# Performance work log

Measured on AMD Instinct MI355X. Metric: run time of the kernel, lower is better.

## Reference

```python
import jax, jax.numpy as jnp
import numpy as np

N, E, B, NC, NCAND, TOK, TITLE, V, GD = 10000, 200000, 64, 50, 5, 38, 30, 50000, 300
H, DH = 20, 20
D = H * DH  # news_dim = 400
NEG = -1e9


def setup_inputs() -> dict:
    key = jax.random.key(0)
    ks = jax.random.split(key, 24)
    s = lambda k, shape, sc=0.02: (jax.random.normal(k, shape, jnp.float32) * sc)
    return dict(
        subgraph_x=jax.random.randint(ks[0], (N, TOK), 0, V, jnp.int32),
        edge_index=jax.random.randint(ks[1], (2, E), 0, N, jnp.int32),
        # -1 marks padded click slots, as in the torch module
        mapping_idx=jax.random.randint(ks[2], (B, NC), -1, N, jnp.int32),
        candidate_news=jax.random.randint(ks[3], (B, NCAND, TOK), 0, V, jnp.int32),
        fake_candidate_news=jax.random.randint(ks[4], (B, NCAND, TOK), 0, V, jnp.int32),
        label=jnp.zeros((B,), jnp.int32),
        glove_emb=s(ks[5], (V, GD), 0.1),
        n_wq=s(ks[6], (GD, D)), n_wk=s(ks[7], (GD, D)), n_wv=s(ks[8], (GD, D)),
        n_wp=s(ks[9], (D, 200)), n_qp=s(ks[10], (200,)),
        ggc_w=s(ks[11], (3, D, D)),
        gru_wih=s(ks[12], (D, 3 * D)), gru_whh=s(ks[13], (D, 3 * D)),
        gru_bih=jnp.zeros((3 * D,), jnp.float32), gru_bhh=jnp.zeros((3 * D,), jnp.float32),
        w_click=s(ks[14], (2 * D, D)), b_click=jnp.zeros((D,), jnp.float32),
        u_wq=s(ks[15], (D, D)), u_wk=s(ks[16], (D, D)), u_wv=s(ks[17], (D, D)),
        u_wp=s(ks[18], (D, 200)), u_qp=s(ks[19], (200,)),
    )


def reference(subgraph_x, edge_index, mapping_idx, candidate_news, fake_candidate_news,
              label, glove_emb, n_wq, n_wk, n_wv, n_wp, n_qp, ggc_w, gru_wih, gru_whh,
              gru_bih, gru_bhh, w_click, b_click, u_wq, u_wk, u_wv, u_wp, u_qp):
    inv_sqrt = 1.0 / np.sqrt(DH).astype(np.float32)

    def news_encode(tokens):  # [..., TITLE] int -> [..., D]
        emb = glove_emb[tokens]                               # [..., T, GD]
        hd = emb.shape[:-1] + (H, DH)
        q = (emb @ n_wq).reshape(hd)
        k = (emb @ n_wk).reshape(hd)
        v = (emb @ n_wv).reshape(hd)
        att = jax.nn.softmax(jnp.einsum('...qhd,...khd->...hqk', q, k) * inv_sqrt, axis=-1)
        out = jnp.einsum('...hqk,...khd->...qhd', att, v).reshape(emb.shape[:-1] + (D,))
        a = jax.nn.softmax(jnp.tanh(out @ n_wp) @ n_qp, axis=-1)  # attention pooling over tokens
        return jnp.einsum('...t,...td->...d', a, out)

    # ---- process_news: encode every node once ----
    x_encoded = news_encode(subgraph_x[:, :TITLE])            # [N, D]
    mask = mapping_idx >= 0                                   # [B, NC]
    midx = jnp.where(mask, mapping_idx, 0)
    clicked_origin = x_encoded[midx] * mask[..., None]        # gather + masked_fill -> [B, NC, D]

    # ---- server: GatedGraphConv(D, num_layers=3, aggr='add') ----
    src, dst = edge_index[0], edge_index[1]
    h = x_encoded
    for l in range(3):
        m = h @ ggc_w[l]
        agg = jax.ops.segment_sum(m[src], dst, num_segments=x_encoded.shape[0])
        gi = agg @ gru_wih + gru_bih
        gh = h @ gru_whh + gru_bhh
        i_r, i_z, i_n = jnp.split(gi, 3, axis=-1)
        h_r, h_z, h_n = jnp.split(gh, 3, axis=-1)
        r = jax.nn.sigmoid(i_r + h_r)
        z = jax.nn.sigmoid(i_z + h_z)
        n = jnp.tanh(i_n + r * h_n)
        h = (1.0 - z) * n + z * h
    clicked_graph = h[midx] * mask[..., None]                 # [B, NC, D]

    # ---- click encoder: combine origin + graph views ----
    clicked_total = jnp.concatenate([clicked_origin, clicked_graph], -1) @ w_click + b_click  # [B,NC,D]

    # ---- user encoder: masked MHSA + masked attention pooling ----
    bsz, nc = clicked_total.shape[:2]
    q = (clicked_total @ u_wq).reshape(bsz, nc, H, DH)
    k = (clicked_total @ u_wk).reshape(bsz, nc, H, DH)
    v = (clicked_total @ u_wv).reshape(bsz, nc, H, DH)
    bias = jnp.where(mask, 0.0, NEG)                          # [B, NC]
    att = jax.nn.softmax(jnp.einsum('bqhd,bkhd->bhqk', q, k) * inv_sqrt + bias[:, None, None, :], axis=-1)
    out = jnp.einsum('bhqk,bkhd->bqhd', att, v).reshape(bsz, nc, D)
    pa = jax.nn.softmax(jnp.tanh(out @ u_wp) @ u_qp + bias, axis=-1)
    user_emb = jnp.einsum('bt,btd->bd', pa, out)              # [B, D]

    # ---- candidate encoding + dot-product scoring ----
    def score_cand(cand):
        c = news_encode(cand[..., :TITLE])                    # [B, NCAND, D]
        return jnp.einsum('bcd,bd->bc', c, user_emb)

    score_real = score_cand(candidate_news)
    score_fake = score_cand(fake_candidate_news)

    # ---- security loss: NCE (cross-entropy) + fake-uniformity penalty ----
    lsm = jax.nn.log_softmax(score_real, axis=-1)
    loss_real = -jnp.mean(jnp.take_along_axis(lsm, label[:, None], axis=1))
    loss_fake = -jnp.mean(jax.nn.log_softmax(score_fake, axis=-1))
    loss = 1.0 * loss_real + 0.5 * loss_fake
    return loss, score_real, score_fake
```

## Files before the change

### kernel.cpp

```cpp
#include <hip/hip_runtime.h>
#include <cmath>

#define NN 10000
#define EE 200000
#define BB 64
#define NCK 50
#define NCAND 5
#define TOKS 38
#define TITLE 30
#define GDIM 300
#define HH 20
#define DHD 20
#define DD 400
#define PP 200

typedef __attribute__((ext_vector_type(8))) short bh8;
typedef __attribute__((ext_vector_type(4))) float f32x4;

__device__ __forceinline__ float bf2f(unsigned short u) {
    return __uint_as_float(((unsigned int)u) << 16);
}
__device__ __forceinline__ unsigned short f2bf(float f) {
    unsigned int u = __float_as_uint(f);
    u += 0x7fffu + ((u >> 16) & 1u);
    return (unsigned short)(u >> 16);
}

__global__ __launch_bounds__(256) void prep_wt(
    const float* __restrict__ wq, const float* __restrict__ wk,
    const float* __restrict__ wv, unsigned short* __restrict__ Wt)
{
    int i = blockIdx.x * 256 + threadIdx.x;
    if (i >= 1200 * 320) return;
    int n = i / 320, k = i % 320;
    int m = n / 400, nn = n % 400;
    const float* W = (m == 0) ? wq : ((m == 1) ? wk : wv);
    float v = (k < GDIM) ? W[(size_t)k * DD + nn] : 0.f;
    Wt[i] = f2bf(v);
}

__global__ __launch_bounds__(256) void prep_wpt(
    const float* __restrict__ wp, unsigned short* __restrict__ wpT)
{
    int i = blockIdx.x * 256 + threadIdx.x;
    if (i >= 208 * 416) return;
    int n = i / 416, k = i % 416;
    float v = (n < PP && k < DD) ? wp[(size_t)k * PP + n] : 0.f;
    wpT[i] = f2bf(v);
}

__global__ __launch_bounds__(256) void prep_wgg(
    const float* __restrict__ ggc, unsigned short* __restrict__ wggT)
{
    int i = blockIdx.x * 256 + threadIdx.x;
    if (i >= 3 * 400 * 424) return;
    int l = i / (400*424), rem = i % (400*424);
    int n = rem / 424, k = rem % 424;
    float v = (k < DD) ? ggc[(size_t)l*DD*DD + (size_t)k*DD + n] : 0.f;
    wggT[i] = f2bf(v);
}

__global__ __launch_bounds__(256) void prep_gruw(
    const float* __restrict__ wih, const float* __restrict__ whh,
    unsigned short* __restrict__ wihT, unsigned short* __restrict__ whhT)
{
    int i = blockIdx.x * 256 + threadIdx.x;
    if (i >= 1200 * 424) return;
    int n = i / 424, k = i % 424;
    wihT[i] = f2bf((k < DD) ? wih[(size_t)k*1200 + n] : 0.f);
    whhT[i] = f2bf((k < DD) ? whh[(size_t)k*1200 + n] : 0.f);
}

__global__ __launch_bounds__(256) void news_enc(
    const int* __restrict__ sub_x,
    const int* __restrict__ cand,
    const int* __restrict__ fcand,
    const float* __restrict__ glove,
    const unsigned short* __restrict__ Wt,
    const unsigned short* __restrict__ wpT,
    const float* __restrict__ qp,
    float* __restrict__ x_enc,
    float* __restrict__ crnc,
    float* __restrict__ cfnc)
{
    __shared__ __align__(16) unsigned short uS[12288];
    __shared__ __align__(16) unsigned short outS[32*408 + 16];
    __shared__ int   tokS[32];
    __shared__ float alphaS[32];

    float* poolP = (float*)uS;

    const int tid  = threadIdx.x;
    const int item = blockIdx.x;
    const int w    = tid >> 6;
    const int lane = tid & 63;
    const int g    = lane >> 4;
    const int l15  = lane & 15;

    const int* tsrc; float* odst;
    if (item < NN) {
        tsrc = sub_x + (size_t)item * TOKS;
        odst = x_enc + (size_t)item * DD;
    } else if (item < NN + BB*NCAND) {
        int li = item - NN;
        tsrc = cand + (size_t)li * TOKS;
        odst = crnc + (size_t)li * DD;
    } else {
        int li = item - NN - BB*NCAND;
        tsrc = fcand + (size_t)li * TOKS;
        odst = cfnc + (size_t)li * DD;
    }

    if (tid < TITLE) tokS[tid] = tsrc[tid];
    for (int i = tid; i < 12288/2; i += 256) ((unsigned int*)uS)[i] = 0u;
    for (int i = tid; i < (32*408+16)/2; i += 256) ((unsigned int*)outS)[i] = 0u;
    __syncthreads();

    for (int i = tid; i < TITLE * 75; i += 256) {
        int t = i / 75, g4 = i % 75;
        const float4 v = *(const float4*)&glove[(size_t)tokS[t] * GDIM + g4 * 4];
        uS[t*328 + g4*4+0] = f2bf(v.x);
        uS[t*328 + g4*4+1] = f2bf(v.y);
        uS[t*328 + g4*4+2] = f2bf(v.z);
        uS[t*328 + g4*4+3] = f2bf(v.w);
    }
    __syncthreads();

    bh8 afr[2][10];
    #pragma unroll
    for (int mt = 0; mt < 2; ++mt)
        #pragma unroll
        for (int ks = 0; ks < 10; ++ks)
            afr[mt][ks] = *(const bh8*)&uS[(mt*16 + l15)*328 + ks*32 + g*8];
    __syncthreads();

    for (int i = tid; i < 12288/2; i += 256) ((unsigned int*)uS)[i] = 0u;
    __syncthreads();

    const float sc = 0.2236067977f;

    for (int hg = 0; hg < 5; ++hg) {
        {
            unsigned short* qme = uS + w*1024;
            for (int i = lane; i < 32*6; i += 64) {
                int r = i / 6, c = 20 + (i % 6) * 2;
                *(unsigned int*)&qme[r*32 + c] = 0u;
            }
        }

        #pragma unroll
        for (int tp = 0; tp < 2; ++tp) {
            const int ta = w*4 + tp*2, tb = ta + 1;
            const bool va_ = (ta < 15), vb_ = (tb < 15);
            const int tca = va_ ? ta : 0, tcb = vb_ ? tb : 0;
            const int ma = tca / 5, loca = tca % 5;
            const int mb = tcb / 5, locb = tcb % 5;
            const unsigned short* wba =
                Wt + (size_t)(ma*400 + hg*80 + loca*16 + l15) * 320;
            const unsigned short* wbb =
                Wt + (size_t)(mb*400 + hg*80 + locb*16 + l15) * 320;
            bh8 ba[10], bbf[10];
            #pragma unroll
            for (int ks = 0; ks < 10; ++ks) {
                ba[ks]  = *(const bh8*)&wba[ks*32 + g*8];
                bbf[ks] = *(const bh8*)&wbb[ks*32 + g*8];
            }
            __builtin_amdgcn_sched_barrier(0);
            f32x4 ca0 = {0.f,0.f,0.f,0.f}, ca1 = {0.f,0.f,0.f,0.f};
            f32x4 cb0 = {0.f,0.f,0.f,0.f}, cb1 = {0.f,0.f,0.f,0.f};
            #pragma unroll
            for (int ks = 0; ks < 10; ++ks) {
                ca0 = __builtin_amdgcn_mfma_f32_16x16x32_bf16(afr[0][ks], ba[ks],  ca0, 0, 0, 0);
                ca1 = __builtin_amdgcn_mfma_f32_16x16x32_bf16(afr[1][ks], ba[ks],  ca1, 0, 0, 0);
                cb0 = __builtin_amdgcn_mfma_f32_16x16x32_bf16(afr[0][ks], bbf[ks], cb0, 0, 0, 0);
                cb1 = __builtin_amdgcn_mfma_f32_16x16x32_bf16(afr[1][ks], bbf[ks], cb1, 0, 0, 0);
            }
            if (va_) {
                const int c2 = loca*16 + l15, h2 = c2 / 20, dloc = c2 % 20;
                unsigned short* qs  = uS + h2*1024;
                unsigned short* ks_ = uS + (4+h2)*1024;
                unsigned short* vs  = uS + (8+h2)*1024;
                #pragma unroll
                for (int r = 0; r < 4; ++r) {
                    int row0 = g*4 + r, row1 = 16 + row0;
                    unsigned short v0 = f2bf(ca0[r]), v1 = f2bf(ca1[r]);
                    if (ma == 0)      { qs[row0*32 + dloc] = v0; qs[row1*32 + dloc] = v1; }
                    else if (ma == 1) { ks_[row0*32 + dloc] = v0; ks_[row1*32 + dloc] = v1; }
                    else              { vs[dloc*32 + row0] = v0; vs[dloc*32 + row1] = v1; }
                }
            }
            if (vb_) {
                const int c2 = locb*16 + l15, h2 = c2 / 20, dloc = c2 % 20;
                unsigned short* qs  = uS + h2*1024;
                unsigned short* ks_ = uS + (4+h2)*1024;
                unsigned short* vs  = uS + (8+h2)*1024;
                #pragma unroll
                for (int r = 0; r < 4; ++r) {
                    int row0 = g*4 + r, row1 = 16 + row0;
                    unsigned short v0 = f2bf(cb0[r]), v1 = f2bf(cb1[r]);
                    if (mb == 0)      { qs[row0*32 + dloc] = v0; qs[row1*32 + dloc] = v1; }
                    else if (mb == 1) { ks_[row0*32 + dloc] = v0; ks_[row1*32 + dloc] = v1; }
                    else              { vs[dloc*32 + row0] = v0; vs[dloc*32 + row1] = v1; }
                }
            }
        }
        __syncthreads();

        {
            unsigned short* qh = uS + w*1024;
            const unsigned short* kh = uS + (4+w)*1024;
            const unsigned short* vh = uS + (8+w)*1024;
            bh8 a0 = *(const bh8*)&qh[l15*32 + g*8];
            bh8 a1 = *(const bh8*)&qh[(16+l15)*32 + g*8];
            bh8 b0 = *(const bh8*)&kh[l15*32 + g*8];
            bh8 b1 = *(const bh8*)&kh[(16+l15)*32 + g*8];
            bh8 vb0 = *(const bh8*)&vh[l15*32 + g*8];
            bh8 vb1 = *(const bh8*)&vh[(16+l15)*32 + g*8];
            f32x4 s00 = {0.f,0.f,0.f,0.f}, s01 = {0.f,0.f,0.f,0.f};
            f32x4 s10 = {0.f,0.f,0.f,0.f}, s11 = {0.f,0.f,0.f,0.f};
            s00 = __builtin_amdgcn_mfma_f32_16x16x32_bf16(a0, b0, s00, 0, 0, 0);
            s01 = __builtin_amdgcn_mfma_f32_16x16x32_bf16(a0, b1, s01, 0, 0, 0);
            s10 = __builtin_amdgcn_mfma_f32_16x16x32_bf16(a1, b0, s10, 0, 0, 0);
            s11 = __builtin_amdgcn_mfma_f32_16x16x32_bf16(a1, b1, s11, 0, 0, 0);
            const float maskv = (l15 >= 14) ? -1e30f : 0.f;
            float sum0[4], sum1[4];
            #pragma unroll
            for (int r = 0; r < 4; ++r) {
                float ea0 = __expf(s00[r]*sc);
                float ea1 = __expf(s01[r]*sc + maskv);
                float eb0 = __expf(s10[r]*sc);
                float eb1 = __expf(s11[r]*sc + maskv);
                int row0 = g*4 + r, row1 = 16 + row0;
                qh[row0*32 + l15]      = f2bf(ea0);
                qh[row0*32 + 16 + l15] = f2bf(ea1);
                qh[row1*32 + l15]      = f2bf(eb0);
                qh[row1*32 + 16 + l15] = f2bf(eb1);
                sum0[r] = ea0 + ea1;
                sum1[r] = eb0 + eb1;
            }
            asm volatile("s_waitcnt lgkmcnt(0)" ::: "memory");
            __builtin_amdgcn_sched_barrier(0);

            bh8 pa0 = *(const bh8*)&qh[l15*32 + g*8];
            bh8 pa1 = *(const bh8*)&qh[(16+l15)*32 + g*8];
            f32x4 o00 = {0.f,0.f,0.f,0.f}, o01 = {0.f,0.f,0.f,0.f};
            f32x4 o10 = {0.f,0.f,0.f,0.f}, o11 = {0.f,0.f,0.f,0.f};
            o00 = __builtin_amdgcn_mfma_f32_16x16x32_bf16(pa0, vb0, o00, 0, 0, 0);
            o01 = __builtin_amdgcn_mfma_f32_16x16x32_bf16(pa0, vb1, o01, 0, 0, 0);
            o10 = __builtin_amdgcn_mfma_f32_16x16x32_bf16(pa1, vb0, o10, 0, 0, 0);
            o11 = __builtin_amdgcn_mfma_f32_16x16x32_bf16(pa1, vb1, o11, 0, 0, 0);
            float inv0[4], inv1[4];
            #pragma unroll
            for (int r = 0; r < 4; ++r) {
                float t0 = sum0[r], t1 = sum1[r];
                #pragma unroll
                for (int mk = 1; mk < 16; mk <<= 1) {
                    t0 += __shfl_xor(t0, mk);
                    t1 += __shfl_xor(t1, mk);
                }
                inv0[r] = 1.f / t0;
                inv1[r] = 1.f / t1;
            }
            const int base = (hg*4 + w) * 20;
            #pragma unroll
            for (int r = 0; r < 4; ++r) {
                int row0 = g*4 + r, row1 = 16 + g*4 + r;
                outS[row0*408 + base + l15] = f2bf(o00[r] * inv0[r]);
                if (l15 < 4) outS[row0*408 + base + 16 + l15] = f2bf(o01[r] * inv0[r]);
                outS[row1*408 + base + l15] = f2bf(o10[r] * inv1[r]);
                if (l15 < 4) outS[row1*408 + base + 16 + l15] = f2bf(o11[r] * inv1[r]);
            }
        }
        __syncthreads();
    }

    for (int i = tid; i < 32*16; i += 256) poolP[i] = 0.f;
    __syncthreads();
    for (int t = w; t < 13; t += 4) {
        const unsigned short* wb = wpT + (size_t)(t*16 + l15) * 416;
        bh8 bfr[13];
        #pragma unroll
        for (int ks = 0; ks < 13; ++ks)
            bfr[ks] = *(const bh8*)&wb[ks*32 + g*8];
        __builtin_amdgcn_sched_barrier(0);
        f32x4 c0 = {0.f,0.f,0.f,0.f}, c1 = {0.f,0.f,0.f,0.f};
        #pragma unroll
        for (int ks = 0; ks < 13; ++ks) {
            bh8 a0 = *(const bh8*)&outS[l15*408 + ks*32 + g*8];
            bh8 a1 = *(const bh8*)&outS[(16+l15)*408 + ks*32 + g*8];
            c0 = __builtin_amdgcn_mfma_f32_16x16x32_bf16(a0, bfr[ks], c0, 0, 0, 0);
            c1 = __builtin_amdgcn_mfma_f32_16x16x32_bf16(a1, bfr[ks], c1, 0, 0, 0);
        }
        int n = t*16 + l15;
        float qpn = (n < PP) ? qp[n] : 0.f;
        #pragma unroll
        for (int r = 0; r < 4; ++r) {
            float v0 = tanhf(c0[r]) * qpn;
            float v1 = tanhf(c1[r]) * qpn;
            #pragma unroll
            for (int mk = 1; mk < 16; mk <<= 1) {
                v0 += __shfl_xor(v0, mk);
                v1 += __shfl_xor(v1, mk);
            }
            if (l15 == 0) {
                poolP[(g*4+r)*16 + t]    = v0;
                poolP[(16+g*4+r)*16 + t] = v1;
            }
        }
    }
    __syncthreads();

    if (tid < 64) {
        float s = -1e30f;
        if (tid < TITLE) {
            s = 0.f;
            for (int t = 0; t < 13; ++t) s += poolP[tid*16 + t];
        }
        float mx = s;
        #pragma unroll
        for (int mk = 1; mk < 64; mk <<= 1) mx = fmaxf(mx, __shfl_xor(mx, mk));
        float e = (tid < TITLE) ? __expf(s - mx) : 0.f;
        float ssum = e;
        #pragma unroll
        for (int mk = 1; mk < 64; mk <<= 1) ssum += __shfl_xor(ssum, mk);
        if (tid < TITLE) alphaS[tid] = e / ssum;
    }
    __syncthreads();
    for (int dd = tid; dd < DD; dd += 256) {
        float a = 0.f;
        for (int t = 0; t < TITLE; ++t) a += alphaS[t] * bf2f(outS[t*408 + dd]);
        odst[dd] = a;
    }
}

__global__ __launch_bounds__(256) void mm_nodes_mfma(
    const float* __restrict__ A, const unsigned short* __restrict__ WT,
    unsigned short* __restrict__ Mo)
{
    __shared__ __align__(16) unsigned short aS[16 * 424];
    const int r0 = blockIdx.x * 16, ny = blockIdx.y, tid = threadIdx.x;
    const int w = tid >> 6, lane = tid & 63, g = lane >> 4, l15 = lane & 15;
    for (int i = tid; i < 16*424; i += 256) {
        int r = i / 424, c = i % 424;
        float v = (c < DD) ? A[(size_t)(r0 + r)*DD + c] : 0.f;
        aS[i] = f2bf(v);
    }
    __syncthreads();
    const int tstart = ny * 13, tcnt = ny ? 12 : 13;
    for (int tt = w; tt < tcnt; tt += 4) {
        int t = tstart + tt;
        const unsigned short* wb = WT + (size_t)(t*16 + l15) * 424;
        f32x4 c0 = {0.f,0.f,0.f,0.f};
        #pragma unroll
        for (int ks = 0; ks < 13; ++ks) {
            bh8 a0 = *(const bh8*)&aS[l15*424 + ks*32 + g*8];
            bh8 b  = *(const bh8*)&wb[ks*32 + g*8];
            c0 = __builtin_amdgcn_mfma_f32_16x16x32_bf16(a0, b, c0, 0, 0, 0);
        }
        int d = t*16 + l15;
        #pragma unroll
        for (int r = 0; r < 4; ++r)
            Mo[(size_t)(r0 + g*4 + r)*DD + d] = f2bf(c0[r]);
    }
}

__global__ __launch_bounds__(256) void count_edges(
    const int* __restrict__ ei, int* __restrict__ cnt)
{
    int e = blockIdx.x * 256 + threadIdx.x;
    if (e < EE) atomicAdd(&cnt[ei[EE + e]], 1);
}

__global__ __launch_bounds__(256) void build_offsets(
    const int* __restrict__ cnt, int* __restrict__ off, int* __restrict__ cursor)
{
    __shared__ int csum[256];
    const int tid = threadIdx.x;
    const int chunk = (NN + 255) / 256;
    int s = 0;
    for (int i = 0; i < chunk; ++i) {
        int idx = tid * chunk + i;
        if (idx < NN) s += cnt[idx];
    }
    csum[tid] = s;
    __syncthreads();
    if (tid == 0) {
        int run = 0;
        for (int i = 0; i < 256; ++i) { int c = csum[i]; csum[i] = run; run += c; }
    }
    __syncthreads();
    int run = csum[tid];
    for (int i = 0; i < chunk; ++i) {
        int idx = tid * chunk + i;
        if (idx < NN) {
            off[idx] = run; cursor[idx] = run;
            run += cnt[idx];
        }
    }
}

__global__ __launch_bounds__(256) void fill_csr(
    const int* __restrict__ ei, int* __restrict__ cursor, int* __restrict__ srclist)
{
    int e = blockIdx.x * 256 + threadIdx.x;
    if (e < EE) {
        int d = ei[EE + e];
        int pos = atomicAdd(&cursor[d], 1);
        srclist[pos] = ei[e];
    }
}

__global__ __launch_bounds__(256) void gather_agg(
    const unsigned short* __restrict__ m, const int* __restrict__ off,
    const int* __restrict__ cnt, const int* __restrict__ srclist,
    float* __restrict__ agg)
{
    __shared__ int sl[128];
    const int node = blockIdx.x, tid = threadIdx.x;
    const int o0 = off[node], deg = cnt[node];
    float acc0 = 0.f, acc1 = 0.f;
    const int d0 = tid, d1 = tid + 256;
    for (int j0 = 0; j0 < deg; j0 += 128) {
        if (tid < 128 && j0 + tid < deg) sl[tid] = srclist[o0 + j0 + tid];
        __syncthreads();
        const int jn = (deg - j0 < 128) ? (deg - j0) : 128;
        for (int j = 0; j < jn; ++j) {
            const unsigned short* mr = &m[(size_t)sl[j] * DD];
            acc0 += bf2f(mr[d0]);
            if (d1 < DD) acc1 += bf2f(mr[d1]);
        }
        __syncthreads();
    }
    agg[(size_t)node * DD + d0] = acc0;
    if (d1 < DD) agg[(size_t)node * DD + d1] = acc1;
}

__global__ __launch_bounds__(256) void gru_step_mfma(
    const float* __restrict__ agg, const float* __restrict__ hin,
    const unsigned short* __restrict__ wihT, const unsigned short* __restrict__ whhT,
    const float* __restrict__ bih, const float* __restrict__ bhh,
    float* __restrict__ hout)
{
    __shared__ __align__(16) unsigned short aggS[16 * 424];
    __shared__ __align__(16) unsigned short hS[16 * 424];
    const int r0 = blockIdx.x * 16, ny = blockIdx.y, tid = threadIdx.x;
    const int w = tid >> 6, lane = tid & 63, g = lane >> 4, l15 = lane & 15;
    for (int i = tid; i < 16*424; i += 256) {
        int r = i / 424, c = i % 424;
        float va = 0.f, vh = 0.f;
        if (c < DD) {
            va = agg[(size_t)(r0 + r)*DD + c];
            vh = hin[(size_t)(r0 + r)*DD + c];
        }
        aggS[i] = f2bf(va); hS[i] = f2bf(vh);
    }
    __syncthreads();
    const int tstart = ny * 13, tcnt = ny ? 12 : 13;
    for (int tt = w; tt < tcnt; tt += 4) {
        int t = tstart + tt;
        int d = t*16 + l15;
        const unsigned short* bri = wihT + (size_t)d * 424;
        const unsigned short* bzi = wihT + (size_t)(400 + d) * 424;
        const unsigned short* bni = wihT + (size_t)(800 + d) * 424;
        const unsigned short* brh = whhT + (size_t)d * 424;
        const unsigned short* bzh = whhT + (size_t)(400 + d) * 424;
        const unsigned short* bnh = whhT + (size_t)(800 + d) * 424;
        f32x4 ir = {0.f,0.f,0.f,0.f}, iz = {0.f,0.f,0.f,0.f}, in_ = {0.f,0.f,0.f,0.f};
        f32x4 hr = {0.f,0.f,0.f,0.f}, hz = {0.f,0.f,0.f,0.f}, hn = {0.f,0.f,0.f,0.f};
        #pragma unroll
        for (int ks = 0; ks < 13; ++ks) {
            bh8 aa = *(const bh8*)&aggS[l15*424 + ks*32 + g*8];
            bh8 ah = *(const bh8*)&hS[l15*424 + ks*32 + g*8];
            bh8 b0 = *(const bh8*)&bri[ks*32 + g*8];
            bh8 b1 = *(const bh8*)&bzi[ks*32 + g*8];
            bh8 b2 = *(const bh8*)&bni[ks*32 + g*8];
            bh8 b3 = *(const bh8*)&brh[ks*32 + g*8];
            bh8 b4 = *(const bh8*)&bzh[ks*32 + g*8];
            bh8 b5 = *(const bh8*)&bnh[ks*32 + g*8];
            ir  = __builtin_amdgcn_mfma_f32_16x16x32_bf16(aa, b0, ir,  0, 0, 0);
            iz  = __builtin_amdgcn_mfma_f32_16x16x32_bf16(aa, b1, iz,  0, 0, 0);
            in_ = __builtin_amdgcn_mfma_f32_16x16x32_bf16(aa, b2, in_, 0, 0, 0);
            hr  = __builtin_amdgcn_mfma_f32_16x16x32_bf16(ah, b3, hr,  0, 0, 0);
            hz  = __builtin_amdgcn_mfma_f32_16x16x32_bf16(ah, b4, hz,  0, 0, 0);
            hn  = __builtin_amdgcn_mfma_f32_16x16x32_bf16(ah, b5, hn,  0, 0, 0);
        }
        float bir = bih[d], biz = bih[400+d], bin = bih[800+d];
        float bhr = bhh[d], bhz = bhh[400+d], bhn = bhh[800+d];
        #pragma unroll
        for (int r = 0; r < 4; ++r) {
            int grow = r0 + g*4 + r;
            float hl = hin[(size_t)grow*DD + d];
            float rg = 1.f/(1.f + __expf(-(ir[r]+bir + hr[r]+bhr)));
            float zg = 1.f/(1.f + __expf(-(iz[r]+biz + hz[r]+bhz)));
            float ng = tanhf(in_[r]+bin + rg*(hn[r]+bhn));
            hout[(size_t)grow*DD + d] = (1.f-zg)*ng + zg*hl;
        }
    }
}

__global__ __launch_bounds__(256) void clicked_mm(
    const int* __restrict__ map, const float* __restrict__ xe,
    const float* __restrict__ hg, const float* __restrict__ wc,
    const float* __restrict__ bc, float* __restrict__ ct)
{
    __shared__ float a[8][2*DD];
    const int r0 = blockIdx.x * 8, tid = threadIdx.x;
    for (int i = tid; i < 8*2*DD; i += 256) {
        int r = i/(2*DD), k = i%(2*DD);
        int mi = map[r0 + r];
        float v = 0.f;
        if (mi >= 0) v = (k < DD) ? xe[(size_t)mi*DD + k] : hg[(size_t)mi*DD + (k-DD)];
        a[r][k] = v;
    }
    __syncthreads();
    for (int d = tid; d < DD; d += 256) {
        float acc[8] = {0,0,0,0,0,0,0,0};
        for (int k = 0; k < 2*DD; ++k) {
            float w = wc[(size_t)k*DD + d];
            #pragma unroll
            for (int r = 0; r < 8; ++r) acc[r] += a[r][k]*w;
        }
        float bb = bc[d];
        #pragma unroll
        for (int r = 0; r < 8; ++r) ct[(size_t)(r0+r)*DD + d] = acc[r] + bb;
    }
}

__global__ __launch_bounds__(256) void user_qkv(
    const float* __restrict__ ct,
    const float* __restrict__ wq, const float* __restrict__ wk, const float* __restrict__ wv,
    float* __restrict__ uq, float* __restrict__ uk, float* __restrict__ uv)
{
    __shared__ float a[8][DD];
    const int r0 = blockIdx.x * 8, tid = threadIdx.x;
    for (int i = tid; i < 8*DD; i += 256)
        a[i/DD][i%DD] = ct[(size_t)(r0 + i/DD)*DD + i%DD];
    __syncthreads();
    for (int d = tid; d < DD; d += 256) {
        float aq[8]={0,0,0,0,0,0,0,0}, ak[8]={0,0,0,0,0,0,0,0}, av[8]={0,0,0,0,0,0,0,0};
        for (int k = 0; k < DD; ++k) {
            float wq_ = wq[(size_t)k*DD + d];
            float wk_ = wk[(size_t)k*DD + d];
            float wv_ = wv[(size_t)k*DD + d];
            #pragma unroll
            for (int r = 0; r < 8; ++r) {
                float x = a[r][k];
                aq[r] += x*wq_; ak[r] += x*wk_; av[r] += x*wv_;
            }
        }
        #pragma unroll
        for (int r = 0; r < 8; ++r) {
            uq[(size_t)(r0+r)*DD + d] = aq[r];
            uk[(size_t)(r0+r)*DD + d] = ak[r];
            uv[(size_t)(r0+r)*DD + d] = av[r];
        }
    }
}

__global__ __launch_bounds__(64) void user_attn(
    const float* __restrict__ uq, const float* __restrict__ uk,
    const float* __restrict__ uv, const int* __restrict__ map,
    float* __restrict__ uo)
{
    const int b = blockIdx.x / HH, h = blockIdx.x % HH, tid = threadIdx.x;
    __shared__ float q[NCK][DHD], k[NCK][DHD], v[NCK][DHD];
    __shared__ float sc[NCK][NCK+2];
    __shared__ float biasl[NCK];
    for (int i = tid; i < NCK*DHD; i += 64) {
        int c = i/DHD, d = i%DHD;
        size_t base = ((size_t)b*NCK + c)*DD + h*DHD + d;
        q[c][d] = uq[base]; k[c][d] = uk[base]; v[c][d] = uv[base];
    }
    for (int i = tid; i < NCK; i += 64)
        biasl[i] = (map[b*NCK + i] >= 0) ? 0.f : -1e9f;
    __syncthreads();
    for (int i = tid; i < NCK*NCK; i += 64) {
        int t = i/NCK, k2 = i%NCK;
        float s = 0.f;
        #pragma unroll
        for (int d4 = 0; d4 < 5; ++d4) {
            const float4 qa = *(const float4*)&q[t][d4*4];
            const float4 kb = *(const float4*)&k[k2][d4*4];
            s += qa.x*kb.x + qa.y*kb.y + qa.z*kb.z + qa.w*kb.w;
        }
        sc[t][k2] = s * 0.2236067977f + biasl[k2];
    }
    __syncthreads();
    if (tid < NCK) {
        float mx = -1e30f;
        for (int k2 = 0; k2 < NCK; ++k2) mx = fmaxf(mx, sc[tid][k2]);
        float ssum = 0.f;
        for (int k2 = 0; k2 < NCK; ++k2) { float e = __expf(sc[tid][k2]-mx); sc[tid][k2] = e; ssum += e; }
        float inv = 1.f/ssum;
        for (int k2 = 0; k2 < NCK; ++k2) sc[tid][k2] *= inv;
    }
    __syncthreads();
    for (int i = tid; i < NCK*DHD; i += 64) {
        int t = i/DHD, d = i%DHD;
        float o = 0.f;
        for (int k2 = 0; k2 < NCK; ++k2) o += sc[t][k2]*v[k2][d];
        uo[((size_t)b*NCK + t)*DD + h*DHD + d] = o;
    }
}

__global__ __launch_bounds__(256) void pool_scores_mfma(
    const float* __restrict__ uo, const unsigned short* __restrict__ uwpT,
    const float* __restrict__ uqp, float* __restrict__ alphaRaw)
{
    __shared__ __align__(16) unsigned short aS[16 * 424];
    __shared__ float poolB[16][16];
    const int r0 = blockIdx.x * 16, tid = threadIdx.x;
    const int w = tid >> 6, lane = tid & 63, g = lane >> 4, l15 = lane & 15;
    for (int i = tid; i < 16*424; i += 256) {
        int r = i / 424, c = i % 424;
        float v = (c < DD) ? uo[(size_t)(r0 + r)*DD + c] : 0.f;
        aS[i] = f2bf(v);
    }
    if (tid < 256) poolB[tid/16][tid%16] = 0.f;
    __syncthreads();
    for (int t = w; t < 13; t += 4) {
        const unsigned short* wb = uwpT + (size_t)(t*16 + l15) * 416;
        bh8 bfr[13];
        #pragma unroll
        for (int ks = 0; ks < 13; ++ks)
            bfr[ks] = *(const bh8*)&wb[ks*32 + g*8];
        __builtin_amdgcn_sched_barrier(0);
        f32x4 c0 = {0.f,0.f,0.f,0.f};
        #pragma unroll
        for (int ks = 0; ks < 13; ++ks) {
            bh8 a0 = *(const bh8*)&aS[l15*424 + ks*32 + g*8];
            c0 = __builtin_amdgcn_mfma_f32_16x16x32_bf16(a0, bfr[ks], c0, 0, 0, 0);
        }
        int n = t*16 + l15;
        float qpn = (n < PP) ? uqp[n] : 0.f;
        #pragma unroll
        for (int r = 0; r < 4; ++r) {
            float v = tanhf(c0[r]) * qpn;
            #pragma unroll
            for (int mk = 1; mk < 16; mk <<= 1) v += __shfl_xor(v, mk);
            if (l15 == 0) poolB[g*4 + r][t] = v;
        }
    }
    __syncthreads();
    if (tid < 16) {
        float s = 0.f;
        for (int t = 0; t < 13; ++t) s += poolB[tid][t];
        alphaRaw[r0 + tid] = s;
    }
}

__global__ __launch_bounds__(256) void user_finalize(
    const float* __restrict__ alphaRaw, const int* __restrict__ map,
    const float* __restrict__ uo, float* __restrict__ user_emb)
{
    const int b = blockIdx.x, tid = threadIdx.x;
    __shared__ float alpha[64];
    if (tid < 64) {
        float a = -1e30f;
        if (tid < NCK)
            a = alphaRaw[b*NCK + tid] + ((map[b*NCK + tid] >= 0) ? 0.f : -1e9f);
        float mx = a;
        #pragma unroll
        for (int mk = 1; mk < 64; mk <<= 1) mx = fmaxf(mx, __shfl_xor(mx, mk));
        float e = (tid < NCK) ? __expf(a - mx) : 0.f;
        float ssum = e;
        #pragma unroll
        for (int mk = 1; mk < 64; mk <<= 1) ssum += __shfl_xor(ssum, mk);
        if (tid < NCK) alpha[tid] = e / ssum;
    }
    __syncthreads();
    for (int d = tid; d < DD; d += 256) {
        float acc = 0.f;
        for (int t = 0; t < NCK; ++t) acc += alpha[t] * uo[((size_t)b*NCK + t)*DD + d];
        user_emb[(size_t)b*DD + d] = acc;
    }
}

__global__ __launch_bounds__(256) void score_loss(
    const float* __restrict__ cr, const float* __restrict__ cf,
    const float* __restrict__ ue, const int* __restrict__ label,
    float* __restrict__ dout)
{
    __shared__ float sr[BB][NCAND], sf[BB][NCAND], red[BB];
    const int tid = threadIdx.x;
    for (int i = tid; i < 2*BB*NCAND; i += 256) {
        int which = i / (BB*NCAND);
        int r = i % (BB*NCAND);
        int b = r / NCAND, c = r % NCAND;
        const float* ce = (which ? cf : cr) + (size_t)r*DD;
        const float* u = ue + (size_t)b*DD;
        float s = 0.f;
        for (int d = 0; d < DD; ++d) s += ce[d]*u[d];
        if (which) sf[b][c] = s; else sr[b][c] = s;
        dout[1 + i] = s;
    }
    __syncthreads();
    if (tid < BB) {
        int b = tid;
        float mr = -1e30f, mf = -1e30f;
        for (int c = 0; c < NCAND; ++c) { mr = fmaxf(mr, sr[b][c]); mf = fmaxf(mf, sf[b][c]); }
        float er = 0.f, ef = 0.f;
        for (int c = 0; c < NCAND; ++c) { er += expf(sr[b][c]-mr); ef += expf(sf[b][c]-mf); }
        float lser = logf(er)+mr, lsef = logf(ef)+mf;
        int lab = label[b]; lab = lab < 0 ? 0 : (lab > NCAND-1 ? NCAND-1 : lab);
        float crb = lser - sr[b][lab];
        float cfb = 0.f;
        for (int c = 0; c < NCAND; ++c) cfb += (lsef - sf[b][c]);
        red[tid] = crb + 0.5f * (cfb / (float)NCAND);
    }
    __syncthreads();
    if (tid == 0) {
        float L = 0.f;
        for (int b = 0; b < BB; ++b) L += red[b];
        dout[0] = L / (float)BB;
    }
}

extern "C" void kernel_launch(void* const* d_in, const int* in_sizes, int n_in,
                              void* d_out, int out_size, void* d_ws, size_t ws_size,
                              hipStream_t stream) {
    (void)in_sizes; (void)n_in; (void)out_size; (void)ws_size;
    const int*   sub_x  = (const int*)d_in[0];
    const int*   edge   = (const int*)d_in[1];
    const int*   mapi   = (const int*)d_in[2];
    const int*   cand   = (const int*)d_in[3];
    const int*   fcand  = (const int*)d_in[4];
    const int*   label  = (const int*)d_in[5];
    const float* glove  = (const float*)d_in[6];
    const float* nwq    = (const float*)d_in[7];
    const float* nwk    = (const float*)d_in[8];
    const float* nwv    = (const float*)d_in[9];
    const float* nwp    = (const float*)d_in[10];
    const float* nqp    = (const float*)d_in[11];
    const float* ggc    = (const float*)d_in[12];
    const float* wih    = (const float*)d_in[13];
    const float* whh    = (const float*)d_in[14];
    const float* bih    = (const float*)d_in[15];
    const float* bhh    = (const float*)d_in[16];
    const float* wclick = (const float*)d_in[17];
    const float* bclick = (const float*)d_in[18];
    const float* uwq    = (const float*)d_in[19];
    const float* uwk    = (const float*)d_in[20];
    const float* uwv    = (const float*)d_in[21];
    const float* uwp    = (const float*)d_in[22];
    const float* uqp    = (const float*)d_in[23];

    float* ws     = (float*)d_ws;
    float* x_enc  = ws;
    float* hbuf   = ws + 4000000;
    float* region = ws + 8000000;
    unsigned short* mbufBF = (unsigned short*)region;
    float* aggbuf = region + 4000000;
    float* ct   = region;
    float* uq   = region + 1280000;
    float* uk   = region + 2560000;
    float* uv   = region + 3840000;
    float* uo   = region + 5120000;
    float* user = region + 6400000;
    float* alphaRaw = region + 6430000;
    int* ibase   = (int*)((char*)d_ws + (size_t)64*1024*1024);
    int* cnt     = ibase;
    int* off     = ibase + 10000;
    int* cursor  = ibase + 20000;
    int* srclist = ibase + 30000;
    unsigned short* Wt   = (unsigned short*)(ws + 17100000);
    unsigned short* wpT  = (unsigned short*)(ws + 17300000);
    unsigned short* wggT = (unsigned short*)(ws + 17400000);
    unsigned short* wihT = (unsigned short*)(ws + 17700000);
    unsigned short* whhT = (unsigned short*)(ws + 18000000);
    unsigned short* uwpT = (unsigned short*)(ws + 18300000);
    float* hbuf2 = ws + 19000000;
    float* crnc  = ws + 23500000;
    float* cfnc  = ws + 23700000;

    prep_wt<<<1500, 256, 0, stream>>>(nwq, nwk, nwv, Wt);
    prep_wpt<<<338, 256, 0, stream>>>(nwp, wpT);
    prep_wpt<<<338, 256, 0, stream>>>(uwp, uwpT);
    prep_wgg<<<(3*400*424 + 255)/256, 256, 0, stream>>>(ggc, wggT);
    prep_gruw<<<(1200*424 + 255)/256, 256, 0, stream>>>(wih, whh, wihT, whhT);

    news_enc<<<NN + 2*BB*NCAND, 256, 0, stream>>>(
        sub_x, cand, fcand, glove, Wt, wpT, nqp, x_enc, crnc, cfnc);

    hipMemsetAsync(cnt, 0, NN*sizeof(int), stream);
    count_edges<<<(EE+255)/256, 256, 0, stream>>>(edge, cnt);
    build_offsets<<<1, 256, 0, stream>>>(cnt, off, cursor);
    fill_csr<<<(EE+255)/256, 256, 0, stream>>>(edge, cursor, srclist);

    const float* hin = x_enc;
    float* houts[3] = {hbuf, hbuf2, hbuf};
    for (int l = 0; l < 3; ++l) {
        mm_nodes_mfma<<<dim3(625,2), 256, 0, stream>>>(hin, wggT + (size_t)l*400*424, mbufBF);
        gather_agg<<<NN, 256, 0, stream>>>(mbufBF, off, cnt, srclist, aggbuf);
        gru_step_mfma<<<dim3(625,2), 256, 0, stream>>>(aggbuf, hin, wihT, whhT, bih, bhh, houts[l]);
        hin = houts[l];
    }

    clicked_mm<<<(BB*NCK)/8, 256, 0, stream>>>(mapi, x_enc, hbuf, wclick, bclick, ct);
    user_qkv<<<(BB*NCK)/8, 256, 0, stream>>>(ct, uwq, uwk, uwv, uq, uk, uv);
    user_attn<<<BB*HH, 64, 0, stream>>>(uq, uk, uv, mapi, uo);
    pool_scores_mfma<<<(BB*NCK)/16, 256, 0, stream>>>(uo, uwpT, uqp, alphaRaw);
    user_finalize<<<BB, 256, 0, stream>>>(alphaRaw, mapi, uo, user);

    score_loss<<<1, 256, 0, stream>>>(crnc, cfnc, user, label, (float*)d_out);
}
```

Measured before the change: 2.519 ms.

## Split news encoder into chunked embed, per-head-group attention and pooling kernels

Replaces the monolithic news encoder with three kernels: an embedding gather stage writing bf16 rows to global memory, a QKV/attention kernel launched per item and head group, and a pooling kernel. Items are processed in four chunks so intermediate buffers stay smaller. The aim is more parallel blocks and lower per-block LDS pressure instead of looping five head groups serially in one block. It adds global memory round trips for embeddings and attention outputs plus extra kernel launches, and re-reads the embedding fragments once per head group.

```diff
diff --git a/kernel.cpp b/kernel.cpp
--- a/kernel.cpp
+++ b/kernel.cpp
@@ -13,6 +13,8 @@
 #define DHD 20
 #define DD 400
 #define PP 200
+#define NITEMS (NN + 2*BB*NCAND)
+#define CHUNK 2660
 
 typedef __attribute__((ext_vector_type(8))) short bh8;
 typedef __attribute__((ext_vector_type(4))) float f32x4;
@@ -71,211 +73,232 @@
     whhT[i] = f2bf((k < DD) ? whh[(size_t)k*1200 + n] : 0.f);
 }
 
-__global__ __launch_bounds__(256) void news_enc(
+__global__ __launch_bounds__(256) void emb_stage(
     const int* __restrict__ sub_x,
     const int* __restrict__ cand,
     const int* __restrict__ fcand,
     const float* __restrict__ glove,
+    int base,
+    unsigned short* __restrict__ embG)
+{
+    __shared__ int tokS[32];
+    const int tid = threadIdx.x, li = blockIdx.x, gi = base + li;
+    const int* tsrc;
+    if (gi < NN)                 tsrc = sub_x + (size_t)gi * TOKS;
+    else if (gi < NN + BB*NCAND) tsrc = cand  + (size_t)(gi - NN) * TOKS;
+    else                         tsrc = fcand + (size_t)(gi - NN - BB*NCAND) * TOKS;
+    if (tid < TITLE) tokS[tid] = tsrc[tid];
+    __syncthreads();
+    unsigned short* od = embG + (size_t)li * 9600;
+    for (int i = tid; i < TITLE * 75; i += 256) {
+        int t = i / 75, g4 = i % 75;
+        const float4 v = *(const float4*)&glove[(size_t)tokS[t] * GDIM + g4 * 4];
+        od[t*320 + g4*4+0] = f2bf(v.x);
+        od[t*320 + g4*4+1] = f2bf(v.y);
+        od[t*320 + g4*4+2] = f2bf(v.z);
+        od[t*320 + g4*4+3] = f2bf(v.w);
+    }
+    for (int i = tid; i < TITLE * 10; i += 256) {
+        int t = i / 10, c = 300 + (i % 10) * 2;
+        *(unsigned int*)&od[t*320 + c] = 0u;
+    }
+}
+
+__global__ __launch_bounds__(256) void news_qkv2(
+    const unsigned short* __restrict__ embG,
     const unsigned short* __restrict__ Wt,
-    const unsigned short* __restrict__ wpT,
-    const float* __restrict__ qp,
-    float* __restrict__ x_enc,
-    float* __restrict__ crnc,
-    float* __restrict__ cfnc)
+    unsigned short* __restrict__ outG)
 {
     __shared__ __align__(16) unsigned short uS[12288];
-    __shared__ __align__(16) unsigned short outS[32*408 + 16];
-    __shared__ int   tokS[32];
-    __shared__ float alphaS[32];
-
-    float* poolP = (float*)uS;
-
     const int tid  = threadIdx.x;
-    const int item = blockIdx.x;
+    const int li   = blockIdx.x;
+    const int hg   = blockIdx.y;
     const int w    = tid >> 6;
     const int lane = tid & 63;
     const int g    = lane >> 4;
     const int l15  = lane & 15;
 
-    const int* tsrc; float* odst;
-    if (item < NN) {
-        tsrc = sub_x + (size_t)item * TOKS;
-        odst = x_enc + (size_t)item * DD;
-    } else if (item < NN + BB*NCAND) {
-        int li = item - NN;
-        tsrc = cand + (size_t)li * TOKS;
-        odst = crnc + (size_t)li * DD;
-    } else {
-        int li = item - NN - BB*NCAND;
-        tsrc = fcand + (size_t)li * TOKS;
-        odst = cfnc + (size_t)li * DD;
-    }
-
-    if (tid < TITLE) tokS[tid] = tsrc[tid];
     for (int i = tid; i < 12288/2; i += 256) ((unsigned int*)uS)[i] = 0u;
-    for (int i = tid; i < (32*408+16)/2; i += 256) ((unsigned int*)outS)[i] = 0u;
-    __syncthreads();
-
-    for (int i = tid; i < TITLE * 75; i += 256) {
-        int t = i / 75, g4 = i % 75;
-        const float4 v = *(const float4*)&glove[(size_t)tokS[t] * GDIM + g4 * 4];
-        uS[t*328 + g4*4+0] = f2bf(v.x);
-        uS[t*328 + g4*4+1] = f2bf(v.y);
-        uS[t*328 + g4*4+2] = f2bf(v.z);
-        uS[t*328 + g4*4+3] = f2bf(v.w);
-    }
-    __syncthreads();
-
+
+    const unsigned short* eb = embG + (size_t)li * 9600;
+    const bh8 zz = {0,0,0,0,0,0,0,0};
+    const bool row1ok = (16 + l15) < TITLE;
+    const int rr1 = row1ok ? (16 + l15) : 0;
     bh8 afr[2][10];
     #pragma unroll
-    for (int mt = 0; mt < 2; ++mt)
-        #pragma unroll
-        for (int ks = 0; ks < 10; ++ks)
-            afr[mt][ks] = *(const bh8*)&uS[(mt*16 + l15)*328 + ks*32 + g*8];
-    __syncthreads();
-
-    for (int i = tid; i < 12288/2; i += 256) ((unsigned int*)uS)[i] = 0u;
+    for (int ks = 0; ks < 10; ++ks) {
+        afr[0][ks] = *(const bh8*)&eb[l15*320 + ks*32 + g*8];
+        bh8 v = *(const bh8*)&eb[rr1*320 + ks*32 + g*8];
+        afr[1][ks] = row1ok ? v : zz;
+    }
     __syncthreads();
 
     const float sc = 0.2236067977f;
 
-    for (int hg = 0; hg < 5; ++hg) {
-        {
-            unsigned short* qme = uS + w*1024;
-            for (int i = lane; i < 32*6; i += 64) {
-                int r = i / 6, c = 20 + (i % 6) * 2;
-                *(unsigned int*)&qme[r*32 + c] = 0u;
-            }
-        }
-
-        #pragma unroll
-        for (int tp = 0; tp < 2; ++tp) {
-            const int ta = w*4 + tp*2, tb = ta + 1;
-            const bool va_ = (ta < 15), vb_ = (tb < 15);
-            const int tca = va_ ? ta : 0, tcb = vb_ ? tb : 0;
-            const int ma = tca / 5, loca = tca % 5;
-            const int mb = tcb / 5, locb = tcb % 5;
-            const unsigned short* wba =
-                Wt + (size_t)(ma*400 + hg*80 + loca*16 + l15) * 320;
-            const unsigned short* wbb =
-                Wt + (size_t)(mb*400 + hg*80 + locb*16 + l15) * 320;
-            bh8 ba[10], bbf[10];
-            #pragma unroll
-            for (int ks = 0; ks < 10; ++ks) {
-                ba[ks]  = *(const bh8*)&wba[ks*32 + g*8];
-                bbf[ks] = *(const bh8*)&wbb[ks*32 + g*8];
-            }
-            __builtin_amdgcn_sched_barrier(0);
-            f32x4 ca0 = {0.f,0.f,0.f,0.f}, ca1 = {0.f,0.f,0.f,0.f};
-            f32x4 cb0 = {0.f,0.f,0.f,0.f}, cb1 = {0.f,0.f,0.f,0.f};
-            #pragma unroll
-            for (int ks = 0; ks < 10; ++ks) {
-                ca0 = __builtin_amdgcn_mfma_f32_16x16x32_bf16(afr[0][ks], ba[ks],  ca0, 0, 0, 0);
-                ca1 = __builtin_amdgcn_mfma_f32_16x16x32_bf16(afr[1][ks], ba[ks],  ca1, 0, 0, 0);
-                cb0 = __builtin_amdgcn_mfma_f32_16x16x32_bf16(afr[0][ks], bbf[ks], cb0, 0, 0, 0);
-                cb1 = __builtin_amdgcn_mfma_f32_16x16x32_bf16(afr[1][ks], bbf[ks], cb1, 0, 0, 0);
-            }
-            if (va_) {
-                const int c2 = loca*16 + l15, h2 = c2 / 20, dloc = c2 % 20;
-                unsigned short* qs  = uS + h2*1024;
-                unsigned short* ks_ = uS + (4+h2)*1024;
-                unsigned short* vs  = uS + (8+h2)*1024;
-                #pragma unroll
-                for (int r = 0; r < 4; ++r) {
-                    int row0 = g*4 + r, row1 = 16 + row0;
-                    unsigned short v0 = f2bf(ca0[r]), v1 = f2bf(ca1[r]);
-                    if (ma == 0)      { qs[row0*32 + dloc] = v0; qs[row1*32 + dloc] = v1; }
-                    else if (ma == 1) { ks_[row0*32 + dloc] = v0; ks_[row1*32 + dloc] = v1; }
-                    else              { vs[dloc*32 + row0] = v0; vs[dloc*32 + row1] = v1; }
-                }
-            }
-            if (vb_) {
-                const int c2 = locb*16 + l15, h2 = c2 / 20, dloc = c2 % 20;
-                unsigned short* qs  = uS + h2*1024;
-                unsigned short* ks_ = uS + (4+h2)*1024;
-                unsigned short* vs  = uS + (8+h2)*1024;
-                #pragma unroll
-                for (int r = 0; r < 4; ++r) {
-                    int row0 = g*4 + r, row1 = 16 + row0;
-                    unsigned short v0 = f2bf(cb0[r]), v1 = f2bf(cb1[r]);
-                    if (mb == 0)      { qs[row0*32 + dloc] = v0; qs[row1*32 + dloc] = v1; }
-                    else if (mb == 1) { ks_[row0*32 + dloc] = v0; ks_[row1*32 + dloc] = v1; }
-                    else              { vs[dloc*32 + row0] = v0; vs[dloc*32 + row1] = v1; }
-                }
-            }
-        }
-        __syncthreads();
-
-        {
-            unsigned short* qh = uS + w*1024;
-            const unsigned short* kh = uS + (4+w)*1024;
-            const unsigned short* vh = uS + (8+w)*1024;
-            bh8 a0 = *(const bh8*)&qh[l15*32 + g*8];
-            bh8 a1 = *(const bh8*)&qh[(16+l15)*32 + g*8];
-            bh8 b0 = *(const bh8*)&kh[l15*32 + g*8];
-            bh8 b1 = *(const bh8*)&kh[(16+l15)*32 + g*8];
-            bh8 vb0 = *(const bh8*)&vh[l15*32 + g*8];
-            bh8 vb1 = *(const bh8*)&vh[(16+l15)*32 + g*8];
-            f32x4 s00 = {0.f,0.f,0.f,0.f}, s01 = {0.f,0.f,0.f,0.f};
-            f32x4 s10 = {0.f,0.f,0.f,0.f}, s11 = {0.f,0.f,0.f,0.f};
-            s00 = __builtin_amdgcn_mfma_f32_16x16x32_bf16(a0, b0, s00, 0, 0, 0);
-            s01 = __builtin_amdgcn_mfma_f32_16x16x32_bf16(a0, b1, s01, 0, 0, 0);
-            s10 = __builtin_amdgcn_mfma_f32_16x16x32_bf16(a1, b0, s10, 0, 0, 0);
-            s11 = __builtin_amdgcn_mfma_f32_16x16x32_bf16(a1, b1, s11, 0, 0, 0);
-            const float maskv = (l15 >= 14) ? -1e30f : 0.f;
-            float sum0[4], sum1[4];
+    #pragma unroll
+    for (int tp = 0; tp < 2; ++tp) {
+        const int ta = w*4 + tp*2, tb = ta + 1;
+        const bool va_ = (ta < 15), vb_ = (tb < 15);
+        const int tca = va_ ? ta : 0, tcb = vb_ ? tb : 0;
+        const int ma = tca / 5, loca = tca % 5;
+        const int mb = tcb / 5, locb = tcb % 5;
+        const unsigned short* wba =
+            Wt + (size_t)(ma*400 + hg*80 + loca*16 + l15) * 320;
+        const unsigned short* wbb =
+            Wt + (size_t)(mb*400 + hg*80 + locb*16 + l15) * 320;
+        bh8 ba[10], bbf[10];
+        #pragma unroll
+        for (int ks = 0; ks < 10; ++ks) {
+            ba[ks]  = *(const bh8*)&wba[ks*32 + g*8];
+            bbf[ks] = *(const bh8*)&wbb[ks*32 + g*8];
+        }
+        __builtin_amdgcn_sched_barrier(0);
+        f32x4 ca0 = {0.f,0.f,0.f,0.f}, ca1 = {0.f,0.f,0.f,0.f};
+        f32x4 cb0 = {0.f,0.f,0.f,0.f}, cb1 = {0.f,0.f,0.f,0.f};
+        #pragma unroll
+        for (int ks = 0; ks < 10; ++ks) {
+            ca0 = __builtin_amdgcn_mfma_f32_16x16x32_bf16(afr[0][ks], ba[ks],  ca0, 0, 0, 0);
+            ca1 = __builtin_amdgcn_mfma_f32_16x16x32_bf16(afr[1][ks], ba[ks],  ca1, 0, 0, 0);
+            cb0 = __builtin_amdgcn_mfma_f32_16x16x32_bf16(afr[0][ks], bbf[ks], cb0, 0, 0, 0);
+            cb1 = __builtin_amdgcn_mfma_f32_16x16x32_bf16(afr[1][ks], bbf[ks], cb1, 0, 0, 0);
+        }
+        if (va_) {
+            const int c2 = loca*16 + l15, h2 = c2 / 20, dloc = c2 % 20;
+            unsigned short* qs  = uS + h2*1024;
+            unsigned short* ks_ = uS + (4+h2)*1024;
+            unsigned short* vs  = uS + (8+h2)*1024;
             #pragma unroll
             for (int r = 0; r < 4; ++r) {
-                float ea0 = __expf(s00[r]*sc);
-                float ea1 = __expf(s01[r]*sc + maskv);
-                float eb0 = __expf(s10[r]*sc);
-                float eb1 = __expf(s11[r]*sc + maskv);
                 int row0 = g*4 + r, row1 = 16 + row0;
-                qh[row0*32 + l15]      = f2bf(ea0);
-                qh[row0*32 + 16 + l15] = f2bf(ea1);
-                qh[row1*32 + l15]      = f2bf(eb0);
-                qh[row1*32 + 16 + l15] = f2bf(eb1);
-                sum0[r] = ea0 + ea1;
-                sum1[r] = eb0 + eb1;
+                unsigned short v0 = f2bf(ca0[r]), v1 = f2bf(ca1[r]);
+                if (ma == 0)      { qs[row0*32 + dloc] = v0; qs[row1*32 + dloc] = v1; }
+                else if (ma == 1) { ks_[row0*32 + dloc] = v0; ks_[row1*32 + dloc] = v1; }
+                else              { vs[dloc*32 + row0] = v0; vs[dloc*32 + row1] = v1; }
             }
-            asm volatile("s_waitcnt lgkmcnt(0)" ::: "memory");
-            __builtin_amdgcn_sched_barrier(0);
-
-            bh8 pa0 = *(const bh8*)&qh[l15*32 + g*8];
-            bh8 pa1 = *(const bh8*)&qh[(16+l15)*32 + g*8];
-            f32x4 o00 = {0.f,0.f,0.f,0.f}, o01 = {0.f,0.f,0.f,0.f};
-            f32x4 o10 = {0.f,0.f,0.f,0.f}, o11 = {0.f,0.f,0.f,0.f};
-            o00 = __builtin_amdgcn_mfma_f32_16x16x32_bf16(pa0, vb0, o00, 0, 0, 0);
-            o01 = __builtin_amdgcn_mfma_f32_16x16x32_bf16(pa0, vb1, o01, 0, 0, 0);
-            o10 = __builtin_amdgcn_mfma_f32_16x16x32_bf16(pa1, vb0, o10, 0, 0, 0);
-            o11 = __builtin_amdgcn_mfma_f32_16x16x32_bf16(pa1, vb1, o11, 0, 0, 0);
-            float inv0[4], inv1[4];
+        }
+        if (vb_) {
+            const int c2 = locb*16 + l15, h2 = c2 / 20, dloc = c2 % 20;
+            unsigned short* qs  = uS + h2*1024;
+            unsigned short* ks_ = uS + (4+h2)*1024;
+            unsigned short* vs  = uS + (8+h2)*1024;
             #pragma unroll
             for (int r = 0; r < 4; ++r) {
-                float t0 = sum0[r], t1 = sum1[r];
-                #pragma unroll
-                for (int mk = 1; mk < 16; mk <<= 1) {
-                    t0 += __shfl_xor(t0, mk);
-                    t1 += __shfl_xor(t1, mk);
-                }
-                inv0[r] = 1.f / t0;
-                inv1[r] = 1.f / t1;
+                int row0 = g*4 + r, row1 = 16 + row0;
+                unsigned short v0 = f2bf(cb0[r]), v1 = f2bf(cb1[r]);
+                if (mb == 0)      { qs[row0*32 + dloc] = v0; qs[row1*32 + dloc] = v1; }
+                else if (mb == 1) { ks_[row0*32 + dloc] = v0; ks_[row1*32 + dloc] = v1; }
+                else              { vs[dloc*32 + row0] = v0; vs[dloc*32 + row1] = v1; }
             }
-            const int base = (hg*4 + w) * 20;
+        }
+    }
+    __syncthreads();
+
+    {
+        unsigned short* qh = uS + w*1024;
+        const unsigned short* kh = uS + (4+w)*1024;
+        const unsigned short* vh = uS + (8+w)*1024;
+        bh8 a0 = *(const bh8*)&qh[l15*32 + g*8];
+        bh8 a1 = *(const bh8*)&qh[(16+l15)*32 + g*8];
+        bh8 b0 = *(const bh8*)&kh[l15*32 + g*8];
+        bh8 b1 = *(const bh8*)&kh[(16+l15)*32 + g*8];
+        bh8 vb0 = *(const bh8*)&vh[l15*32 + g*8];
+        bh8 vb1 = *(const bh8*)&vh[(16+l15)*32 + g*8];
+        f32x4 s00 = {0.f,0.f,0.f,0.f}, s01 = {0.f,0.f,0.f,0.f};
+        f32x4 s10 = {0.f,0.f,0.f,0.f}, s11 = {0.f,0.f,0.f,0.f};
+        s00 = __builtin_amdgcn_mfma_f32_16x16x32_bf16(a0, b0, s00, 0, 0, 0);
+        s01 = __builtin_amdgcn_mfma_f32_16x16x32_bf16(a0, b1, s01, 0, 0, 0);
+        s10 = __builtin_amdgcn_mfma_f32_16x16x32_bf16(a1, b0, s10, 0, 0, 0);
+        s11 = __builtin_amdgcn_mfma_f32_16x16x32_bf16(a1, b1, s11, 0, 0, 0);
+        const float maskv = (l15 >= 14) ? -1e30f : 0.f;
+        float sum0[4], sum1[4];
+        #pragma unroll
+        for (int r = 0; r < 4; ++r) {
+            float ea0 = __expf(s00[r]*sc);
+            float ea1 = __expf(s01[r]*sc + maskv);
+            float eb0 = __expf(s10[r]*sc);
+            float eb1 = __expf(s11[r]*sc + maskv);
+            int row0 = g*4 + r, row1 = 16 + row0;
+            qh[row0*32 + l15]      = f2bf(ea0);
+            qh[row0*32 + 16 + l15] = f2bf(ea1);
+            qh[row1*32 + l15]      = f2bf(eb0);
+            qh[row1*32 + 16 + l15] = f2bf(eb1);
+            sum0[r] = ea0 + ea1;
+            sum1[r] = eb0 + eb1;
+        }
+        asm volatile("s_waitcnt lgkmcnt(0)" ::: "memory");
+        __builtin_amdgcn_sched_barrier(0);
+
+        bh8 pa0 = *(const bh8*)&qh[l15*32 + g*8];
+        bh8 pa1 = *(const bh8*)&qh[(16+l15)*32 + g*8];
+        f32x4 o00 = {0.f,0.f,0.f,0.f}, o01 = {0.f,0.f,0.f,0.f};
+        f32x4 o10 = {0.f,0.f,0.f,0.f}, o11 = {0.f,0.f,0.f,0.f};
+        o00 = __builtin_amdgcn_mfma_f32_16x16x32_bf16(pa0, vb0, o00, 0, 0, 0);
+        o01 = __builtin_amdgcn_mfma_f32_16x16x32_bf16(pa0, vb1, o01, 0, 0, 0);
+        o10 = __builtin_amdgcn_mfma_f32_16x16x32_bf16(pa1, vb0, o10, 0, 0, 0);
+        o11 = __builtin_amdgcn_mfma_f32_16x16x32_bf16(pa1, vb1, o11, 0, 0, 0);
+        float inv0[4], inv1[4];
+        #pragma unroll
+        for (int r = 0; r < 4; ++r) {
+            float t0 = sum0[r], t1 = sum1[r];
             #pragma unroll
-            for (int r = 0; r < 4; ++r) {
-                int row0 = g*4 + r, row1 = 16 + g*4 + r;
-                outS[row0*408 + base + l15] = f2bf(o00[r] * inv0[r]);
-                if (l15 < 4) outS[row0*408 + base + 16 + l15] = f2bf(o01[r] * inv0[r]);
-                outS[row1*408 + base + l15] = f2bf(o10[r] * inv1[r]);
-                if (l15 < 4) outS[row1*408 + base + 16 + l15] = f2bf(o11[r] * inv1[r]);
+            for (int mk = 1; mk < 16; mk <<= 1) {
+                t0 += __shfl_xor(t0, mk);
+                t1 += __shfl_xor(t1, mk);
             }
-        }
-        __syncthreads();
-    }
-
-    for (int i = tid; i < 32*16; i += 256) poolP[i] = 0.f;
-    __syncthreads();
+            inv0[r] = 1.f / t0;
+            inv1[r] = 1.f / t1;
+        }
+        unsigned short* od = outG + (size_t)li * 12000;
+        const int base = (hg*4 + w) * 20;
+        #pragma unroll
+        for (int r = 0; r < 4; ++r) {
+            int row0 = g*4 + r, row1 = 16 + g*4 + r;
+            od[row0*400 + base + l15] = f2bf(o00[r] * inv0[r]);
+            if (l15 < 4) od[row0*400 + base + 16 + l15] = f2bf(o01[r] * inv0[r]);
+            if (row1 < TITLE) {
+                od[row1*400 + base + l15] = f2bf(o10[r] * inv1[r]);
+                if (l15 < 4) od[row1*400 + base + 16 + l15] = f2bf(o11[r] * inv1[r]);
+            }
+        }
+    }
+}
+
+__global__ __launch_bounds__(256) void news_pool(
+    const unsigned short* __restrict__ outG,
+    const unsigned short* __restrict__ wpT,
+    const float* __restrict__ qp,
+    int base,
+    float* __restrict__ x_enc,
+    float* __restrict__ crnc,
+    float* __restrict__ cfnc)
+{
+    __shared__ __align__(16) unsigned short outS[32*408 + 16];
+    __shared__ float poolP[32][16];
+    __shared__ float alphaS[32];
+
+    const int tid  = threadIdx.x;
+    const int li   = blockIdx.x;
+    const int gi   = base + li;
+    const int w    = tid >> 6;
+    const int lane = tid & 63;
+    const int g    = lane >> 4;
+    const int l15  = lane & 15;
+
+    float* odst;
+    if (gi < NN)                 odst = x_enc + (size_t)gi * DD;
+    else if (gi < NN + BB*NCAND) odst = crnc + (size_t)(gi - NN) * DD;
+    else                         odst = cfnc + (size_t)(gi - NN - BB*NCAND) * DD;
+
+    for (int i = tid; i < (32*408+16)/2; i += 256) ((unsigned int*)outS)[i] = 0u;
+    __syncthreads();
+    const unsigned int* src = (const unsigned int*)(outG + (size_t)li * 12000);
+    for (int i = tid; i < TITLE * 200; i += 256) {
+        int r = i / 200, c2 = (i % 200) * 2;
+        *(unsigned int*)&outS[r*408 + c2] = src[i];
+    }
+    for (int i = tid; i < 32*16; i += 256) poolP[i/16][i%16] = 0.f;
+    __syncthreads();
+
     for (int t = w; t < 13; t += 4) {
         const unsigned short* wb = wpT + (size_t)(t*16 + l15) * 416;
         bh8 bfr[13];
@@ -303,8 +326,8 @@
                 v1 += __shfl_xor(v1, mk);
             }
             if (l15 == 0) {
-                poolP[(g*4+r)*16 + t]    = v0;
-                poolP[(16+g*4+r)*16 + t] = v1;
+                poolP[g*4+r][t]    = v0;
+                poolP[16+g*4+r][t] = v1;
             }
         }
     }
@@ -314,7 +337,7 @@
         float s = -1e30f;
         if (tid < TITLE) {
             s = 0.f;
-            for (int t = 0; t < 13; ++t) s += poolP[tid*16 + t];
+            for (int t = 0; t < 13; ++t) s += poolP[tid][t];
         }
         float mx = s;
         #pragma unroll
@@ -772,6 +795,8 @@
     float* hbuf2 = ws + 19000000;
     float* crnc  = ws + 23500000;
     float* cfnc  = ws + 23700000;
+    unsigned short* embG = (unsigned short*)(ws + 24000000);
+    unsigned short* outG = (unsigned short*)(ws + 37000000);
 
     prep_wt<<<1500, 256, 0, stream>>>(nwq, nwk, nwv, Wt);
     prep_wpt<<<338, 256, 0, stream>>>(nwp, wpT);
@@ -779,8 +804,11 @@
     prep_wgg<<<(3*400*424 + 255)/256, 256, 0, stream>>>(ggc, wggT);
     prep_gruw<<<(1200*424 + 255)/256, 256, 0, stream>>>(wih, whh, wihT, whhT);
 
-    news_enc<<<NN + 2*BB*NCAND, 256, 0, stream>>>(
-        sub_x, cand, fcand, glove, Wt, wpT, nqp, x_enc, crnc, cfnc);
+    for (int c = 0; c < 4; ++c) {
+        emb_stage<<<CHUNK, 256, 0, stream>>>(sub_x, cand, fcand, glove, c*CHUNK, embG);
+        news_qkv2<<<dim3(CHUNK, 5), 256, 0, stream>>>(embG, Wt, outG);
+        news_pool<<<CHUNK, 256, 0, stream>>>(outG, wpT, nqp, c*CHUNK, x_enc, crnc, cfnc);
+    }
 
     hipMemsetAsync(cnt, 0, NN*sizeof(int), stream);
     count_edges<<<(EE+255)/256, 256, 0, stream>>>(edge, cnt);
```

Measured after the change: 3.019 ms. 1.2x slower.
